# Optimization experiments

Hardware: AMD Instinct MI355X
Metric: run time of the kernel (lower is better)

The kernel has to match this reference:

```python
import jax, jax.numpy as jnp
import numpy as np

B, S, D, H, E, K = 4, 1024, 1024, 4096, 8, 2
CAPACITY_FACTOR = 2.0
T = B * S
CAP = int(T * CAPACITY_FACTOR * K / E)  # 2048


def setup_inputs() -> dict:
    key = jax.random.key(0)
    ks = jax.random.split(key, 6)
    std = 0.02
    return {
        "x": jax.random.normal(ks[0], (B, S, D), dtype=jnp.float32),
        "router_w": jax.random.normal(ks[1], (E, D), dtype=jnp.float32) * std,
        "w1": jax.random.normal(ks[2], (E, D, H), dtype=jnp.float32) * std,
        "b1": jnp.zeros((E, H), dtype=jnp.float32),
        "w2": jax.random.normal(ks[3], (E, H, D), dtype=jnp.float32) * std,
        "b2": jnp.zeros((E, D), dtype=jnp.float32),
    }


def reference(x, router_w, w1, b1, w2, b2):
    # Router (eval mode: no logit noise, no dropout)
    logits = jnp.einsum("bsd,ed->bse", x, router_w)            # [B,S,E]
    probs = jax.nn.softmax(logits, axis=-1)
    topk_p, topk_i = jax.lax.top_k(probs, K)                   # [B,S,K]
    gates = topk_p / jnp.sum(topk_p, axis=-1, keepdims=True)

    xt = x.reshape(T, D)                                        # tokens
    eidx = topk_i.reshape(T * K)                                # expert per slot
    g = gates.reshape(T * K)
    tok = jnp.arange(T * K) // K                                # token id per slot

    # position of each slot within its expert (first-come-first-served capacity)
    oh = jax.nn.one_hot(eidx, E, dtype=jnp.int32)               # [T*K, E]
    pos = jnp.sum((jnp.cumsum(oh, axis=0) - 1) * oh, axis=1)    # [T*K]
    keep = pos < CAP
    pos_c = jnp.where(keep, pos, CAP)                           # overflow -> padding row

    # dispatch: gather tokens into per-expert buffers [E, CAP, D]
    buf = jnp.zeros((E, CAP + 1, D), x.dtype).at[eidx, pos_c].set(xt[tok])
    inp = buf[:, :CAP]

    # per-expert FFN (exact-erf GELU matches torch nn.GELU default)
    h = jax.nn.gelu(jnp.einsum("ecd,edh->ech", inp, w1) + b1[:, None, :],
                    approximate=False)
    out_e = jnp.einsum("ech,eho->eco", h, w2) + b2[:, None, :]  # [E,CAP,D]

    # combine: gather back to slots, weight by gates, sum over k per token
    gathered = out_e[eidx, jnp.minimum(pos_c, CAP - 1)]         # [T*K, D]
    wslot = g * keep.astype(x.dtype)
    out = (gathered * wslot[:, None]).reshape(T, K, D).sum(axis=1).reshape(B, S, D)

    # load-balancing loss
    router_prob_per_expert = probs.mean(axis=(0, 1))            # [E]
    expert_usage = oh.sum(axis=0).astype(x.dtype) / (T * K)
    lb_loss = jnp.sum(router_prob_per_expert * expert_usage) * E
    return out, lb_loss
```

## Files before the change

kernel.cpp:

```cpp
#include <hip/hip_runtime.h>
#include <cstdint>
#include <cstddef>

#define TDIM 4096
#define DDIM 1024
#define HDIM 4096
#define EDIM 8
#define CAPD 2048
#define NSLOT 8192
#define NROUTERBLK 1024

typedef _Float16 f16;
typedef _Float16 f16x2 __attribute__((ext_vector_type(2)));
typedef _Float16 f16x4 __attribute__((ext_vector_type(4)));
typedef _Float16 f16x8 __attribute__((ext_vector_type(8)));
typedef float f32x4 __attribute__((ext_vector_type(4)));

__device__ __forceinline__ void gload16(const void* g, void* l) {
  __builtin_amdgcn_global_load_lds(
      (const __attribute__((address_space(1))) unsigned int*)g,
      (__attribute__((address_space(3))) unsigned int*)l, 16, 0, 0);
}

__device__ __forceinline__ float gelu_fast(float x) {
  float y = 1.5957691216057308f * (x + 0.044715f * x * x * x);
  y = fminf(y, 60.f);
  float e = __expf(y);
  return x * e * __builtin_amdgcn_rcpf(e + 1.f);
}

__global__ __launch_bounds__(256, 8)
void transpose2_cvt(const float* __restrict__ w1, f16* __restrict__ w1t,
                    const float* __restrict__ w2, f16* __restrict__ w2t) {
  __shared__ __align__(128) char smem[16384];
  const int b = blockIdx.x;
  const int half = b >> 13, within = b & 8191;
  const int e = within >> 10, tile = within & 1023;
  const float* src; f16* dst; int R, C, rt, ct;
  if (half == 0) { src = w1; dst = w1t; R = DDIM; C = HDIM; ct = tile & 63; rt = tile >> 6; }
  else           { src = w2; dst = w2t; R = HDIM; C = DDIM; ct = tile & 15; rt = tile >> 4; }
  const int tid = threadIdx.x, wv = tid >> 6;
  const int r0 = rt * 64, c0 = ct * 64;
  const float* s = src + (size_t)e * R * C + (size_t)r0 * C + c0;
  f16* d = dst + (size_t)e * R * C + (size_t)c0 * R + r0;
  #pragma unroll
  for (int i = 0; i < 4; ++i) {
    const int chunk = i * 256 + tid;
    const int row = chunk >> 4, s4 = chunk & 15;
    const int sl = (s4 & 8) | ((s4 ^ (row >> 3)) & 7);
    gload16(s + (size_t)row * C + sl * 4, smem + i * 4096 + wv * 1024);
  }
  __syncthreads();
  #pragma unroll
  for (int it = 0; it < 2; ++it) {
    const int idx = it * 256 + tid;
    const int c = idx >> 3, w = idx & 7;
    const int slotc = ((c >> 2) & 8) | (((c >> 2) ^ w) & 7);
    const int cb4 = (c & 3) * 4;
    f16x8 o;
    #pragma unroll
    for (int j = 0; j < 8; ++j) {
      const float v = *(const float*)(smem + (8 * w + j) * 256 + slotc * 16 + cb4);
      o[j] = (f16)v;
    }
    *(f16x8*)(d + (size_t)c * R + 8 * w) = o;
  }
}

__global__ void router_k(const float* __restrict__ x, const float* __restrict__ rw,
                         int* __restrict__ eidx, float* __restrict__ gates,
                         float* __restrict__ bps) {
  __shared__ float lrw[EDIM * DDIM];
  __shared__ float wps[4][EDIM];
  const int tid = threadIdx.x, lane = tid & 63, wv = tid >> 6;
  for (int i = tid; i < EDIM * DDIM; i += 256) lrw[i] = rw[i];
  __syncthreads();
  const int t = blockIdx.x * 4 + wv;
  float acc[EDIM];
  #pragma unroll
  for (int e = 0; e < EDIM; ++e) acc[e] = 0.f;
  const float* xr = x + (size_t)t * DDIM;
  #pragma unroll
  for (int j = 0; j < DDIM / 64; ++j) {
    float xv = xr[j * 64 + lane];
    #pragma unroll
    for (int e = 0; e < EDIM; ++e) acc[e] += xv * lrw[e * DDIM + j * 64 + lane];
  }
  #pragma unroll
  for (int off = 32; off >= 1; off >>= 1) {
    #pragma unroll
    for (int e = 0; e < EDIM; ++e) acc[e] += __shfl_xor(acc[e], off);
  }
  float mx = acc[0];
  #pragma unroll
  for (int e = 1; e < EDIM; ++e) mx = fmaxf(mx, acc[e]);
  float p[EDIM], s = 0.f;
  #pragma unroll
  for (int e = 0; e < EDIM; ++e) { p[e] = expf(acc[e] - mx); s += p[e]; }
  float inv = 1.f / s;
  #pragma unroll
  for (int e = 0; e < EDIM; ++e) p[e] *= inv;
  int i1 = 0; float p1 = p[0];
  #pragma unroll
  for (int e = 1; e < EDIM; ++e) if (p[e] > p1) { p1 = p[e]; i1 = e; }
  int i2 = (i1 == 0) ? 1 : 0; float p2 = p[i2];
  #pragma unroll
  for (int e = 0; e < EDIM; ++e) if (e != i1 && p[e] > p2) { p2 = p[e]; i2 = e; }
  float gs = 1.f / (p1 + p2);
  if (lane == 0) {
    eidx[2 * t] = i1; eidx[2 * t + 1] = i2;
    gates[2 * t] = p1 * gs; gates[2 * t + 1] = p2 * gs;
    #pragma unroll
    for (int e = 0; e < EDIM; ++e) wps[wv][e] = p[e];
  }
  __syncthreads();
  if (tid < EDIM)
    bps[blockIdx.x * EDIM + tid] = wps[0][tid] + wps[1][tid] + wps[2][tid] + wps[3][tid];
}

__global__ void count_k(const int* __restrict__ eidx, int* __restrict__ cc) {
  __shared__ int h[EDIM];
  const int tid = threadIdx.x;
  if (tid < EDIM) h[tid] = 0;
  __syncthreads();
  atomicAdd(&h[eidx[blockIdx.x * 256 + tid]], 1);
  __syncthreads();
  if (tid < EDIM) cc[blockIdx.x * EDIM + tid] = h[tid];
}

__global__ void scan_k(const int* __restrict__ cc, const float* __restrict__ bps,
                       int* __restrict__ cb, int* __restrict__ counts,
                       int* __restrict__ rowsNeeded, float* __restrict__ lb_out) {
  __shared__ float red[32][EDIM];
  __shared__ int cnt_s[EDIM];
  const int tid = threadIdx.x;
  const int e = tid & 7, g = tid >> 3;
  float s = 0.f;
  for (int j = 0; j < 32; ++j) s += bps[(g + 32 * j) * EDIM + e];
  red[g][e] = s;
  __syncthreads();
  for (int st = 16; st >= 1; st >>= 1) {
    if (g < st) red[g][e] += red[g + st][e];
    __syncthreads();
  }
  if (tid < EDIM) {
    int base = 0;
    for (int c = 0; c < 32; ++c) { cb[c * EDIM + tid] = base; base += cc[c * EDIM + tid]; }
    counts[tid] = base;
    rowsNeeded[tid] = base < CAPD ? base : CAPD;
    cnt_s[tid] = base;
  }
  __syncthreads();
  if (tid == 0) {
    float lb = 0.f;
    for (int ee = 0; ee < EDIM; ++ee)
      lb += (red[0][ee] / (float)TDIM) * ((float)cnt_s[ee] / (float)NSLOT);
    lb_out[0] = lb * (float)EDIM;
  }
}

__global__ void pos_k(const int* __restrict__ eidx, const float* __restrict__ gates,
                      const int* __restrict__ cb, int* __restrict__ posa,
                      float* __restrict__ wslot) {
  __shared__ int wcnt[4][EDIM];
  const int tid = threadIdx.x, lane = tid & 63, wv = tid >> 6;
  const int slot = blockIdx.x * 256 + tid;
  const int e = eidx[slot];
  const unsigned long long below = (1ull << lane) - 1ull;
  int wavepos = 0;
  #pragma unroll
  for (int ee = 0; ee < EDIM; ++ee) {
    unsigned long long m = __ballot(e == ee);
    if (lane == 0) wcnt[wv][ee] = __popcll(m);
    if (e == ee) wavepos = __popcll(m & below);
  }
  __syncthreads();
  int off = 0;
  for (int w = 0; w < wv; ++w) off += wcnt[w][e];
  const int pos = cb[blockIdx.x * EDIM + e] + off + wavepos;
  posa[slot] = pos;
  wslot[slot] = (pos < CAPD) ? gates[slot] : 0.f;
}

__global__ void scatter2_k(const float* __restrict__ x, const int* __restrict__ eidx,
                           const int* __restrict__ posa, f16* __restrict__ buf) {
  const int t = blockIdx.x, lane = threadIdx.x;
  const int s0 = 2 * t, s1 = 2 * t + 1;
  const int p0 = posa[s0], p1 = posa[s1];
  const int e0 = eidx[s0], e1 = eidx[s1];
  const float4* src = (const float4*)(x + (size_t)t * DDIM);
  f16x8* d0 = (f16x8*)(buf + ((size_t)e0 * CAPD + p0) * DDIM);
  f16x8* d1 = (f16x8*)(buf + ((size_t)e1 * CAPD + p1) * DDIM);
  const bool w0 = p0 < CAPD, w1 = p1 < CAPD;
  #pragma unroll
  for (int j = 0; j < 2; ++j) {
    float4 a = src[j * 128 + lane * 2];
    float4 b = src[j * 128 + lane * 2 + 1];
    f16x8 o;
    o[0] = (f16)a.x; o[1] = (f16)a.y; o[2] = (f16)a.z; o[3] = (f16)a.w;
    o[4] = (f16)b.x; o[5] = (f16)b.y; o[6] = (f16)b.z; o[7] = (f16)b.w;
    if (w0) d0[j * 64 + lane] = o;
    if (w1) d1[j * 64 + lane] = o;
  }
}

#define STAGE(hh, g) do { \
    const f16* s_ = sP[hh] + (g) * 64; \
    char* d_ = smem + (hh) * 8192 + wv * 1024; \
    gload16(s_, d_); \
    gload16(s_ + (size_t)32 * LD, d_ + 4096); \
  } while (0)

template<int KLEN, int LD, int N, int GELU, int NTH, int NKS, int NMT>
__global__ __launch_bounds__(256, 4)
void gemm128s(const f16* __restrict__ A, const f16* __restrict__ Bt,
              const float* __restrict__ bias, f16* __restrict__ C, size_t pstride,
              const int* __restrict__ rowsNeeded) {
  constexpr int NTT = KLEN / 64;
  __shared__ __align__(128) char smem[32768];
  const int wg = blockIdx.x;
  const int e = wg & 7;
  const int r = wg >> 3;
  const int ntl = r % NTH;
  const int ks = (r / NTH) % NKS;
  const int mt = (r / (NTH * NKS)) % NMT;
  const int nth = r / (NTH * NKS * NMT);
  const int nt = nth * NTH + ntl;
  if (mt * 128 >= rowsNeeded[e]) return;
  const int tid = threadIdx.x, lane = tid & 63, wv = tid >> 6;
  const int wr = wv >> 1, wc = wv & 1;
  const int ro = lane & 15, q4 = (lane >> 4) * 4;
  const int ko0b = (lane >> 4) * 16;
  const f16* aBase = A + ((size_t)e * CAPD + (size_t)mt * 128) * LD + (size_t)ks * KLEN;
  const f16* bBase = Bt + ((size_t)e * N + (size_t)nt * 128) * LD + (size_t)ks * KLEN;
  const int row0 = tid >> 3;
  const int sw0 = ((tid & 7) ^ (row0 & 7)) * 8;

  const f16* sP[4];
  sP[0] = aBase + (size_t)row0 * LD + sw0;
  sP[1] = sP[0] + (size_t)64 * LD;
  sP[2] = bBase + (size_t)row0 * LD + sw0;
  sP[3] = sP[2] + (size_t)64 * LD;

  int aoffs[4][2], boffs[4][2];
  #pragma unroll
  for (int m = 0; m < 4; ++m)
    #pragma unroll
    for (int k = 0; k < 2; ++k) {
      const int rh = wr * 64 + m * 16 + ro;
      aoffs[m][k] = rh * 128 + ((k * 64 + ko0b) ^ ((rh & 7) << 4));
      const int rb = wc * 64 + m * 16 + ro;
      boffs[m][k] = 16384 + rb * 128 + ((k * 64 + ko0b) ^ ((rb & 7) << 4));
    }

  f32x4 acc[4][4];
  #pragma unroll
  for (int m = 0; m < 4; ++m)
    #pragma unroll
    for (int n = 0; n < 4; ++n) acc[m][n] = (f32x4){0.f, 0.f, 0.f, 0.f};

  #pragma unroll 1
  for (int t = 0; t < NTT; ++t) {
    STAGE(0, t); STAGE(1, t); STAGE(2, t); STAGE(3, t);
    __syncthreads();
    f16x8 af[4][2], bf[4][2];
    #pragma unroll
    for (int m = 0; m < 4; ++m)
      #pragma unroll
      for (int k = 0; k < 2; ++k) {
        af[m][k] = *(const f16x8*)(smem + aoffs[m][k]);
        bf[m][k] = *(const f16x8*)(smem + boffs[m][k]);
      }
    #pragma unroll
    for (int k = 0; k < 2; ++k)
      #pragma unroll
      for (int m = 0; m < 4; ++m)
        #pragma unroll
        for (int n = 0; n < 4; ++n)
          acc[m][n] = __builtin_amdgcn_mfma_f32_16x16x32_f16(af[m][k], bf[n][k], acc[m][n], 0, 0, 0);
    __syncthreads();
  }

  float bv[4];
  #pragma unroll
  for (int n = 0; n < 4; ++n)
    bv[n] = (ks == 0) ? bias[e * N + nt * 128 + wc * 64 + n * 16 + ro] : 0.f;
  f16* Ct = (f16*)(smem + wv * 8192);
  #pragma unroll
  for (int m = 0; m < 4; ++m)
    #pragma unroll
    for (int n = 0; n < 4; ++n)
      #pragma unroll
      for (int i = 0; i < 4; ++i) {
        const int row = m * 16 + q4 + i;
        float v = acc[m][n][i] + bv[n];
        if (GELU) v = gelu_fast(v);
        *(f16*)((char*)Ct + row * 128 + (((n * 16 + ro) * 2) ^ (((row >> 2) & 3) << 5))) = (f16)v;
      }
  asm volatile("s_waitcnt lgkmcnt(0)" ::: "memory");
  __builtin_amdgcn_sched_barrier(0);
  f16* Cp = C + (size_t)ks * pstride;
  const size_t crow0 = (size_t)e * CAPD + mt * 128 + wr * 64;
  const int ccol0 = nt * 128 + wc * 64;
  #pragma unroll
  for (int j = 0; j < 8; ++j) {
    const int idx = j * 64 + lane;
    const int rr = idx >> 3, c2 = (idx & 7) * 16;
    f16x8 v = *(const f16x8*)((const char*)Ct + rr * 128 + (c2 ^ (((rr >> 2) & 3) << 5)));
    *(f16x8*)(Cp + (crow0 + rr) * N + ccol0 + (idx & 7) * 8) = v;
  }
}

__global__ void combine_k(const f16* __restrict__ pA, const f16* __restrict__ pB,
                          const int* __restrict__ eidx, const int* __restrict__ posa,
                          const float* __restrict__ wslot, float* __restrict__ out) {
  const int t = blockIdx.x, tid = threadIdx.x;
  const int s0 = 2 * t, s1 = 2 * t + 1;
  const int e0 = eidx[s0], e1 = eidx[s1];
  int p0 = posa[s0]; p0 = p0 < CAPD - 1 ? p0 : CAPD - 1;
  int p1 = posa[s1]; p1 = p1 < CAPD - 1 ? p1 : CAPD - 1;
  const float g0 = wslot[s0], g1 = wslot[s1];
  const size_t o0 = ((size_t)e0 * CAPD + p0) * DDIM;
  const size_t o1 = ((size_t)e1 * CAPD + p1) * DDIM;
  const f16x2* r0a = (const f16x2*)(pA + o0);
  const f16x2* r0b = (const f16x2*)(pB + o0);
  const f16x2* r1a = (const f16x2*)(pA + o1);
  const f16x2* r1b = (const f16x2*)(pB + o1);
  float2* o = (float2*)(out + (size_t)t * DDIM);
  #pragma unroll
  for (int j = tid; j < DDIM / 2; j += 256) {
    f16x2 a0 = r0a[j], a1 = r0b[j], b0 = r1a[j], b1 = r1b[j];
    o[j] = make_float2(
        g0 * ((float)a0.x + (float)a1.x) + g1 * ((float)b0.x + (float)b1.x),
        g0 * ((float)a0.y + (float)a1.y) + g1 * ((float)b0.y + (float)b1.y));
  }
}

extern "C" void kernel_launch(void* const* d_in, const int* in_sizes, int n_in,
                              void* d_out, int out_size, void* d_ws, size_t ws_size,
                              hipStream_t stream) {
  (void)in_sizes; (void)n_in; (void)out_size; (void)ws_size;
  const float* x  = (const float*)d_in[0];
  const float* rw = (const float*)d_in[1];
  const float* w1 = (const float*)d_in[2];
  const float* b1 = (const float*)d_in[3];
  const float* w2 = (const float*)d_in[4];
  const float* b2 = (const float*)d_in[5];
  float* out = (float*)d_out;

  char* ws = (char*)d_ws;
  size_t off = 0;
  auto alloc = [&](size_t b) { void* p = ws + off; off += (b + 255) & ~(size_t)255; return p; };
  f16* w1t   = (f16*)alloc((size_t)EDIM * DDIM * HDIM * 2);
  f16* w2t   = (f16*)alloc((size_t)EDIM * DDIM * HDIM * 2);
  f16* buf   = (f16*)alloc((size_t)EDIM * CAPD * DDIM * 2);
  f16* hbuf  = (f16*)alloc((size_t)EDIM * CAPD * HDIM * 2);
  const size_t PSTRIDE = (size_t)EDIM * CAPD * DDIM;
  f16* outeA = (f16*)alloc(PSTRIDE * 2);
  f16* outeB = (f16*)alloc(PSTRIDE * 2);
  int*   eidx   = (int*)alloc(NSLOT * 4);
  int*   posa   = (int*)alloc(NSLOT * 4);
  float* gatesA = (float*)alloc(NSLOT * 4);
  float* wslotA = (float*)alloc(NSLOT * 4);
  int*   cc     = (int*)alloc(32 * EDIM * 4);
  int*   cb     = (int*)alloc(32 * EDIM * 4);
  int*   counts = (int*)alloc(EDIM * 4);
  int*   rowsN  = (int*)alloc(EDIM * 4);
  float* bps    = (float*)alloc(NROUTERBLK * EDIM * 4);
  (void)outeB;

  transpose2_cvt<<<16384, 256, 0, stream>>>(w1, w1t, w2, w2t);

  router_k<<<NROUTERBLK, 256, 0, stream>>>(x, rw, eidx, gatesA, bps);
  count_k<<<32, 256, 0, stream>>>(eidx, cc);
  scan_k<<<1, 256, 0, stream>>>(cc, bps, cb, counts, rowsN, out + (size_t)TDIM * DDIM);
  pos_k<<<32, 256, 0, stream>>>(eidx, gatesA, cb, posa, wslotA);
  scatter2_k<<<TDIM, 64, 0, stream>>>(x, eidx, posa, buf);

  gemm128s<DDIM, DDIM, HDIM, 1, 16, 1, 16><<<4096, 256, 0, stream>>>(
      buf, w1t, b1, hbuf, 0, rowsN);

  gemm128s<HDIM / 2, HDIM, DDIM, 0, 8, 2, 16><<<2048, 256, 0, stream>>>(
      hbuf, w2t, b2, outeA, PSTRIDE, rowsN);

  combine_k<<<TDIM, 256, 0, stream>>>(outeA, outeA + PSTRIDE, eidx, posa, wslotA, out);
}
```

Measured before the change: 293.7 us.

## Use 128x128 tiles with f16 LDS staging in weight transpose-convert kernel

The weight transpose/convert kernel now processes 128x128 tiles per block instead of 64x64, using a quarter as many blocks. Values are converted to f16 before being written to LDS with an XOR swizzle, rather than staging fp32 through async global-to-LDS loads. The goal is larger contiguous writes per column and less per-block overhead in this memory-bound pass. In exchange, LDS use doubles and occupancy is lower, and the explicit register loads replace the async LDS path.

```diff
diff --git a/kernel.cpp b/kernel.cpp
--- a/kernel.cpp
+++ b/kernel.cpp
@@ -29,40 +29,41 @@
   return x * e * __builtin_amdgcn_rcpf(e + 1.f);
 }
 
-__global__ __launch_bounds__(256, 8)
+__global__ __launch_bounds__(256, 4)
 void transpose2_cvt(const float* __restrict__ w1, f16* __restrict__ w1t,
                     const float* __restrict__ w2, f16* __restrict__ w2t) {
-  __shared__ __align__(128) char smem[16384];
+  __shared__ __align__(128) char smem[32768];
   const int b = blockIdx.x;
-  const int half = b >> 13, within = b & 8191;
-  const int e = within >> 10, tile = within & 1023;
-  const float* src; f16* dst; int R, C, rt, ct;
-  if (half == 0) { src = w1; dst = w1t; R = DDIM; C = HDIM; ct = tile & 63; rt = tile >> 6; }
-  else           { src = w2; dst = w2t; R = HDIM; C = DDIM; ct = tile & 15; rt = tile >> 4; }
-  const int tid = threadIdx.x, wv = tid >> 6;
-  const int r0 = rt * 64, c0 = ct * 64;
+  const float* src; f16* dst; int R, C, rt, ct, e;
+  if (b < 2048) {
+    src = w1; dst = w1t; R = DDIM; C = HDIM;
+    e = b >> 8; const int rem = b & 255; ct = rem & 31; rt = rem >> 5;
+  } else {
+    const int b2 = b - 2048;
+    src = w2; dst = w2t; R = HDIM; C = DDIM;
+    e = b2 >> 8; const int rem = b2 & 255; ct = rem & 7; rt = rem >> 3;
+  }
+  const int tid = threadIdx.x;
+  const int r0 = rt * 128, c0 = ct * 128;
   const float* s = src + (size_t)e * R * C + (size_t)r0 * C + c0;
   f16* d = dst + (size_t)e * R * C + (size_t)c0 * R + r0;
   #pragma unroll
-  for (int i = 0; i < 4; ++i) {
-    const int chunk = i * 256 + tid;
-    const int row = chunk >> 4, s4 = chunk & 15;
-    const int sl = (s4 & 8) | ((s4 ^ (row >> 3)) & 7);
-    gload16(s + (size_t)row * C + sl * 4, smem + i * 4096 + wv * 1024);
-  }
-  __syncthreads();
-  #pragma unroll
-  for (int it = 0; it < 2; ++it) {
+  for (int i = 0; i < 16; ++i) {
+    const int idx = i * 256 + tid;
+    const int row = idx >> 5, c4 = (idx & 31) * 4;
+    float4 v = *(const float4*)(s + (size_t)row * C + c4);
+    f16x4 o; o[0] = (f16)v.x; o[1] = (f16)v.y; o[2] = (f16)v.z; o[3] = (f16)v.w;
+    *(f16x4*)(smem + row * 256 + ((c4 * 2) ^ ((row & 7) << 4))) = o;
+  }
+  __syncthreads();
+  #pragma unroll
+  for (int it = 0; it < 8; ++it) {
     const int idx = it * 256 + tid;
-    const int c = idx >> 3, w = idx & 7;
-    const int slotc = ((c >> 2) & 8) | (((c >> 2) ^ w) & 7);
-    const int cb4 = (c & 3) * 4;
+    const int c = idx >> 4, w = idx & 15;
     f16x8 o;
     #pragma unroll
-    for (int j = 0; j < 8; ++j) {
-      const float v = *(const float*)(smem + (8 * w + j) * 256 + slotc * 16 + cb4);
-      o[j] = (f16)v;
-    }
+    for (int j = 0; j < 8; ++j)
+      o[j] = *(const f16*)(smem + (8 * w + j) * 256 + ((c * 2) ^ (j << 4)));
     *(f16x8*)(d + (size_t)c * R + 8 * w) = o;
   }
 }
@@ -369,7 +370,7 @@
   float* bps    = (float*)alloc(NROUTERBLK * EDIM * 4);
   (void)outeB;
 
-  transpose2_cvt<<<16384, 256, 0, stream>>>(w1, w1t, w2, w2t);
+  transpose2_cvt<<<4096, 256, 0, stream>>>(w1, w1t, w2, w2t);
 
   router_k<<<NROUTERBLK, 256, 0, stream>>>(x, rw, eidx, gatesA, bps);
   count_k<<<32, 256, 0, stream>>>(eidx, cc);
```

After: 298.0 us. No clear change (+1.5%).

## Fuse weight fp32-to-fp16 transpose into GEMM B-tile staging

Applied to the files above, without the earlier changes.

Removes the separate transpose/convert kernel that wrote fp16 transposed copies of w1 and w2. The GEMM now reads the fp32 weights directly, converts them to fp16 in registers and writes them transposed into LDS with a new swizzle. This saves one full read-write pass over both weight tensors. In exchange, fp32 weight traffic inside the GEMM doubles and B staging becomes synchronous register loads instead of async global-to-LDS loads. The n-tile grouping (NTH) is also halved.

```diff
diff --git a/kernel.cpp b/kernel.cpp
--- a/kernel.cpp
+++ b/kernel.cpp
@@ -27,44 +27,6 @@
   y = fminf(y, 60.f);
   float e = __expf(y);
   return x * e * __builtin_amdgcn_rcpf(e + 1.f);
-}
-
-__global__ __launch_bounds__(256, 8)
-void transpose2_cvt(const float* __restrict__ w1, f16* __restrict__ w1t,
-                    const float* __restrict__ w2, f16* __restrict__ w2t) {
-  __shared__ __align__(128) char smem[16384];
-  const int b = blockIdx.x;
-  const int half = b >> 13, within = b & 8191;
-  const int e = within >> 10, tile = within & 1023;
-  const float* src; f16* dst; int R, C, rt, ct;
-  if (half == 0) { src = w1; dst = w1t; R = DDIM; C = HDIM; ct = tile & 63; rt = tile >> 6; }
-  else           { src = w2; dst = w2t; R = HDIM; C = DDIM; ct = tile & 15; rt = tile >> 4; }
-  const int tid = threadIdx.x, wv = tid >> 6;
-  const int r0 = rt * 64, c0 = ct * 64;
-  const float* s = src + (size_t)e * R * C + (size_t)r0 * C + c0;
-  f16* d = dst + (size_t)e * R * C + (size_t)c0 * R + r0;
-  #pragma unroll
-  for (int i = 0; i < 4; ++i) {
-    const int chunk = i * 256 + tid;
-    const int row = chunk >> 4, s4 = chunk & 15;
-    const int sl = (s4 & 8) | ((s4 ^ (row >> 3)) & 7);
-    gload16(s + (size_t)row * C + sl * 4, smem + i * 4096 + wv * 1024);
-  }
-  __syncthreads();
-  #pragma unroll
-  for (int it = 0; it < 2; ++it) {
-    const int idx = it * 256 + tid;
-    const int c = idx >> 3, w = idx & 7;
-    const int slotc = ((c >> 2) & 8) | (((c >> 2) ^ w) & 7);
-    const int cb4 = (c & 3) * 4;
-    f16x8 o;
-    #pragma unroll
-    for (int j = 0; j < 8; ++j) {
-      const float v = *(const float*)(smem + (8 * w + j) * 256 + slotc * 16 + cb4);
-      o[j] = (f16)v;
-    }
-    *(f16x8*)(d + (size_t)c * R + 8 * w) = o;
-  }
 }
 
 __global__ void router_k(const float* __restrict__ x, const float* __restrict__ rw,
@@ -204,16 +166,30 @@
   }
 }
 
-#define STAGE(hh, g) do { \
+#define STAGE_A(hh, g) do { \
     const f16* s_ = sP[hh] + (g) * 64; \
     char* d_ = smem + (hh) * 8192 + wv * 1024; \
     gload16(s_, d_); \
-    gload16(s_ + (size_t)32 * LD, d_ + 4096); \
+    gload16(s_ + (size_t)32 * LDA, d_ + 4096); \
   } while (0)
 
-template<int KLEN, int LD, int N, int GELU, int NTH, int NKS, int NMT>
+#define STAGE_B(g) do { \
+    const float* bs_ = bBase + (size_t)((g) * 64 + k0b) * LDB + n0b; \
+    float4 rr[8]; \
+    _Pragma("unroll") for (int j_ = 0; j_ < 8; ++j_) \
+      rr[j_] = *(const float4*)(bs_ + (size_t)j_ * LDB); \
+    _Pragma("unroll") for (int i_ = 0; i_ < 4; ++i_) { \
+      f16x8 o_; \
+      _Pragma("unroll") for (int j_ = 0; j_ < 8; ++j_) \
+        o_[j_] = (f16)(((const float*)&rr[j_])[i_]); \
+      const int row_ = n0b + i_; \
+      *(f16x8*)(smem + 16384 + row_ * 128 + 16 * ((k0b >> 3) ^ ((row_ >> 2) & 7))) = o_; \
+    } \
+  } while (0)
+
+template<int KLEN, int LDA, int LDB, int N, int GELU, int NTH, int NKS, int NMT>
 __global__ __launch_bounds__(256, 4)
-void gemm128s(const f16* __restrict__ A, const f16* __restrict__ Bt,
+void gemm128d(const f16* __restrict__ A, const float* __restrict__ Bw,
               const float* __restrict__ bias, f16* __restrict__ C, size_t pstride,
               const int* __restrict__ rowsNeeded) {
   constexpr int NTT = KLEN / 64;
@@ -231,16 +207,16 @@
   const int wr = wv >> 1, wc = wv & 1;
   const int ro = lane & 15, q4 = (lane >> 4) * 4;
   const int ko0b = (lane >> 4) * 16;
-  const f16* aBase = A + ((size_t)e * CAPD + (size_t)mt * 128) * LD + (size_t)ks * KLEN;
-  const f16* bBase = Bt + ((size_t)e * N + (size_t)nt * 128) * LD + (size_t)ks * KLEN;
+  const f16* aBase = A + ((size_t)e * CAPD + (size_t)mt * 128) * LDA + (size_t)ks * KLEN;
+  const float* bBase = Bw + ((size_t)e * KLEN * NKS + (size_t)ks * KLEN) * LDB + nt * 128;
   const int row0 = tid >> 3;
   const int sw0 = ((tid & 7) ^ (row0 & 7)) * 8;
-
-  const f16* sP[4];
-  sP[0] = aBase + (size_t)row0 * LD + sw0;
-  sP[1] = sP[0] + (size_t)64 * LD;
-  sP[2] = bBase + (size_t)row0 * LD + sw0;
-  sP[3] = sP[2] + (size_t)64 * LD;
+  const int n0b = (tid & 31) * 4;
+  const int k0b = (tid >> 5) * 8;
+
+  const f16* sP[2];
+  sP[0] = aBase + (size_t)row0 * LDA + sw0;
+  sP[1] = sP[0] + (size_t)64 * LDA;
 
   int aoffs[4][2], boffs[4][2];
   #pragma unroll
@@ -250,7 +226,7 @@
       const int rh = wr * 64 + m * 16 + ro;
       aoffs[m][k] = rh * 128 + ((k * 64 + ko0b) ^ ((rh & 7) << 4));
       const int rb = wc * 64 + m * 16 + ro;
-      boffs[m][k] = 16384 + rb * 128 + ((k * 64 + ko0b) ^ ((rb & 7) << 4));
+      boffs[m][k] = 16384 + rb * 128 + ((k * 64 + ko0b) ^ (((rb >> 2) & 7) << 4));
     }
 
   f32x4 acc[4][4];
@@ -261,7 +237,8 @@
 
   #pragma unroll 1
   for (int t = 0; t < NTT; ++t) {
-    STAGE(0, t); STAGE(1, t); STAGE(2, t); STAGE(3, t);
+    STAGE_A(0, t); STAGE_A(1, t);
+    STAGE_B(t);
     __syncthreads();
     f16x8 af[4][2], bf[4][2];
     #pragma unroll
@@ -351,8 +328,6 @@
   char* ws = (char*)d_ws;
   size_t off = 0;
   auto alloc = [&](size_t b) { void* p = ws + off; off += (b + 255) & ~(size_t)255; return p; };
-  f16* w1t   = (f16*)alloc((size_t)EDIM * DDIM * HDIM * 2);
-  f16* w2t   = (f16*)alloc((size_t)EDIM * DDIM * HDIM * 2);
   f16* buf   = (f16*)alloc((size_t)EDIM * CAPD * DDIM * 2);
   f16* hbuf  = (f16*)alloc((size_t)EDIM * CAPD * HDIM * 2);
   const size_t PSTRIDE = (size_t)EDIM * CAPD * DDIM;
@@ -369,19 +344,17 @@
   float* bps    = (float*)alloc(NROUTERBLK * EDIM * 4);
   (void)outeB;
 
-  transpose2_cvt<<<16384, 256, 0, stream>>>(w1, w1t, w2, w2t);
-
   router_k<<<NROUTERBLK, 256, 0, stream>>>(x, rw, eidx, gatesA, bps);
   count_k<<<32, 256, 0, stream>>>(eidx, cc);
   scan_k<<<1, 256, 0, stream>>>(cc, bps, cb, counts, rowsN, out + (size_t)TDIM * DDIM);
   pos_k<<<32, 256, 0, stream>>>(eidx, gatesA, cb, posa, wslotA);
   scatter2_k<<<TDIM, 64, 0, stream>>>(x, eidx, posa, buf);
 
-  gemm128s<DDIM, DDIM, HDIM, 1, 16, 1, 16><<<4096, 256, 0, stream>>>(
-      buf, w1t, b1, hbuf, 0, rowsN);
-
-  gemm128s<HDIM / 2, HDIM, DDIM, 0, 8, 2, 16><<<2048, 256, 0, stream>>>(
-      hbuf, w2t, b2, outeA, PSTRIDE, rowsN);
+  gemm128d<DDIM, DDIM, HDIM, HDIM, 1, 8, 1, 16><<<4096, 256, 0, stream>>>(
+      buf, w1, b1, hbuf, 0, rowsN);
+
+  gemm128d<HDIM / 2, HDIM, DDIM, DDIM, 0, 4, 2, 16><<<2048, 256, 0, stream>>>(
+      hbuf, w2, b2, outeA, PSTRIDE, rowsN);
 
   combine_k<<<TDIM, 256, 0, stream>>>(outeA, outeA + PSTRIDE, eidx, posa, wslotA, out);
 }
```

After: 307.2 us. +4.6%, slower.
